# Kernel tuning notes

Measured on AMD Instinct MI355X. Metric: run time of the kernel, lower is better.

## Reference

```python
import jax, jax.numpy as jnp
import numpy as np

B, T, H, I, O, R = 64, 1024, 1024, 8, 8, 4
NOISE_STD, ALPHA = 0.05, 0.2


def setup_inputs() -> dict:
    key = jax.random.key(0)
    ks = jax.random.split(key, 6)
    return {
        "x": jax.random.normal(ks[0], (B, T, I), jnp.float32),
        "noise": jax.random.normal(ks[1], (B, T, H), jnp.float32),
        "wi": jax.random.normal(ks[2], (I, H), jnp.float32),
        "si": jnp.ones((I,), jnp.float32),
        "m": jax.random.normal(ks[3], (H, R), jnp.float32),
        "n": jax.random.normal(ks[4], (H, R), jnp.float32),
        "b": jnp.zeros((H,), jnp.float32),
        "wo": jax.random.normal(ks[5], (H, O), jnp.float32) / H,
        "so": jnp.ones((O,), jnp.float32),
        "h0": jnp.zeros((H,), jnp.float32),
    }


def reference(x, noise, wi, si, m, n, b, wo, so, h0):
    hidden = h0.shape[0]
    batch = x.shape[0]
    wi_full = wi * si[:, None]          # (I, H): (wi.T * si).T
    wo_full = wo * so                   # (H, O)
    h_init = jnp.broadcast_to(h0, (batch, hidden))
    r_init = jnp.tanh(h_init)           # non_linearity(initial_states)
    # precompute input drive for all steps: (B,T,H) -> scan over time-major
    u = jnp.einsum('bti,ih->tbh', x, wi_full)
    noise_t = jnp.transpose(noise, (1, 0, 2))  # (T,B,H)

    def step(carry, inp):
        h, r = carry
        u_i, nz_i = inp
        rec = (r @ n) @ m.T / hidden                    # low-rank recurrence
        h = h + NOISE_STD * nz_i + ALPHA * (-h + rec + u_i)
        r = jnp.tanh(h + b)
        out = h @ wo_full                               # identity output nonlin
        return (h, r), out

    _, outs = jax.lax.scan(step, (h_init, r_init), (u, noise_t))
    return jnp.transpose(outs, (1, 0, 2))  # (B,T,O)
```

## Files before the change

kernel.cpp:

```cpp
#include <hip/hip_runtime.h>

#define BB 64
#define TT 1024
#define HH 1024
#define II 8
#define OO 8
#define RRK 4
#define NOISE_STD 0.05f
#define ALPHA 0.2f

typedef float v4f __attribute__((ext_vector_type(4)));

#define C2E 2.885390081777927f

template<int CTRL, int RM>
__device__ __forceinline__ float dpp_add(float acc, float src) {
    int s = __builtin_amdgcn_update_dpp(0, __float_as_int(src), CTRL, RM, 0xF, true);
    return acc + __int_as_float(s);
}

__device__ __forceinline__ float wave_sum(float x) {
    x = dpp_add<0xB1, 0xF>(x, x);
    x = dpp_add<0x4E, 0xF>(x, x);
    x = dpp_add<0x141, 0xF>(x, x);
    x = dpp_add<0x140, 0xF>(x, x);
    x = dpp_add<0x142, 0xA>(x, x);
    x = dpp_add<0x143, 0xC>(x, x);
    return x;
}

__device__ __forceinline__ float rl63(float x) {
    return __int_as_float(__builtin_amdgcn_readlane(__float_as_int(x), 63));
}

__device__ __forceinline__ float tanh_from_l2x(float l2x) {
    float e = __builtin_amdgcn_exp2f(l2x);
    float r = __builtin_amdgcn_rcpf(e + 1.0f);
    return fmaf(-2.0f, r, 1.0f);
}

__device__ __forceinline__ void block_sync_lds() {
    asm volatile("s_waitcnt lgkmcnt(0)\n\ts_barrier" ::: "memory");
}

__device__ __forceinline__ void lds_fence() {
    asm volatile("s_waitcnt lgkmcnt(0)" ::: "memory");
}


__global__ __launch_bounds__(256)
void pre_d_kernel(const float* __restrict__ x, const float* __restrict__ noise,
                  const float* __restrict__ wi, const float* __restrict__ si,
                  const float* __restrict__ wo, const float* __restrict__ so,
                  float* __restrict__ d, float* __restrict__ sbase) {
    __shared__ __align__(16) float red[2][8][4][8];

    const int tid  = threadIdx.x;
    const int wave = tid >> 6;
    const int lane = tid & 63;
    const int e0   = tid << 2;

    v4f wia4[II];
    #pragma unroll
    for (int i = 0; i < II; ++i)
        wia4[i] = (ALPHA * si[i]) * *(const v4f*)(wi + (size_t)i * HH + e0);

    float woa[4][OO];
    #pragma unroll
    for (int e = 0; e < 4; ++e) {
        const float4 a4 = *(const float4*)(wo + (e0 + e) * OO);
        const float4 b4 = *(const float4*)(wo + (e0 + e) * OO + 4);
        woa[e][0] = a4.x * so[0]; woa[e][1] = a4.y * so[1];
        woa[e][2] = a4.z * so[2]; woa[e][3] = a4.w * so[3];
        woa[e][4] = b4.x * so[4]; woa[e][5] = b4.y * so[5];
        woa[e][6] = b4.z * so[6]; woa[e][7] = b4.w * so[7];
    }

    const int row0 = blockIdx.x * 32;
    float4 nz[8], nzn[8];
    #pragma unroll
    for (int j = 0; j < 8; ++j)
        nz[j] = *(const float4*)(noise + (size_t)(row0 + j) * HH + e0);

    #pragma unroll
    for (int ph = 0; ph < 4; ++ph) {
        const int cur   = ph & 1;
        const int rbase = row0 + ph * 8;

        if (ph < 3) {
            #pragma unroll
            for (int j = 0; j < 8; ++j)
                nzn[j] = *(const float4*)(noise + (size_t)(rbase + 8 + j) * HH + e0);
        }

        #pragma unroll
        for (int j = 0; j < 8; ++j) {
            const int row = rbase + j;
            const float4 xr0 = *(const float4*)(x + (size_t)row * II);
            const float4 xr1 = *(const float4*)(x + (size_t)row * II + 4);
            v4f u = xr0.x * wia4[0];
            u += xr0.y * wia4[1];  u += xr0.z * wia4[2];
            u += xr0.w * wia4[3];  u += xr1.x * wia4[4];
            u += xr1.y * wia4[5];  u += xr1.z * wia4[6];
            u += xr1.w * wia4[7];
            v4f d4 = u;
            d4.x = fmaf(NOISE_STD, nz[j].x, d4.x);
            d4.y = fmaf(NOISE_STD, nz[j].y, d4.y);
            d4.z = fmaf(NOISE_STD, nz[j].z, d4.z);
            d4.w = fmaf(NOISE_STD, nz[j].w, d4.w);
            *(v4f*)(d + (size_t)row * HH + e0) = d4;

            float op[OO];
            #pragma unroll
            for (int o = 0; o < OO; ++o)
                op[o] = fmaf(d4.x, woa[0][o], fmaf(d4.y, woa[1][o],
                        fmaf(d4.z, woa[2][o], d4.w * woa[3][o])));
            #pragma unroll
            for (int o = 0; o < OO; ++o) op[o] = wave_sum(op[o]);
            if (lane == 63) {
                *(float4*)&red[cur][j][wave][0] = make_float4(op[0], op[1], op[2], op[3]);
                *(float4*)&red[cur][j][wave][4] = make_float4(op[4], op[5], op[6], op[7]);
            }
        }
        block_sync_lds();
        if (tid < 64) {
            const int j = tid >> 3, o = tid & 7;
            sbase[(rbase + j) * OO + o] = (red[cur][j][0][o] + red[cur][j][1][o]) +
                                          (red[cur][j][2][o] + red[cur][j][3][o]);
        }
        #pragma unroll
        for (int j = 0; j < 8; ++j) nz[j] = nzn[j];
    }
}

__global__ __launch_bounds__(64, 1)
void rnn_d_kernel(const float* __restrict__ d, const float* __restrict__ sbase,
                  const float* __restrict__ mM, const float* __restrict__ nM,
                  const float* __restrict__ bv, const float* __restrict__ wo,
                  const float* __restrict__ so, const float* __restrict__ h0,
                  float* __restrict__ out) {
    __shared__ __align__(16) float lds_sb[TT * OO];
    __shared__ __align__(16) float lds_v[TT * RRK];
    __shared__ __align__(16) float amy[40];
    __shared__ float chs[8][OO];

    const int lane = threadIdx.x;
    const int b    = blockIdx.x;
    const int e0   = lane << 4;
    const int oc   = lane & 7;

    {
        const float4* ss = (const float4*)(sbase + (size_t)b * (TT * OO));
        float4* dsb = (float4*)lds_sb;
        #pragma unroll
        for (int k = 0; k < 32; ++k)
            dsb[k * 64 + lane] = ss[k * 64 + lane];
    }

    v4f mag[4][RRK];
    {
        const float cs = ALPHA / (float)HH;
        #pragma unroll
        for (int g = 0; g < 4; ++g) {
            v4f m0 = cs * *(const v4f*)(mM + (size_t)(e0 + g*4 + 0) * RRK);
            v4f m1 = cs * *(const v4f*)(mM + (size_t)(e0 + g*4 + 1) * RRK);
            v4f m2 = cs * *(const v4f*)(mM + (size_t)(e0 + g*4 + 2) * RRK);
            v4f m3 = cs * *(const v4f*)(mM + (size_t)(e0 + g*4 + 3) * RRK);
            #pragma unroll
            for (int q = 0; q < RRK; ++q)
                mag[g][q] = (v4f){m0[q], m1[q], m2[q], m3[q]};
        }
    }
    v4f h[4], r[4], tb[4];
    #pragma unroll
    for (int g = 0; g < 4; ++g) {
        h[g]  = *(const v4f*)(h0 + e0 + g * 4);
        tb[g] = C2E * *(const v4f*)(bv + e0 + g * 4);
        const v4f tg = C2E * h[g];
        r[g].x = tanh_from_l2x(tg.x); r[g].y = tanh_from_l2x(tg.y);
        r[g].z = tanh_from_l2x(tg.z); r[g].w = tanh_from_l2x(tg.w);
    }

    {
        float acc[40];
        #pragma unroll
        for (int k = 0; k < 40; ++k) acc[k] = 0.0f;
        float so8[OO];
        #pragma unroll
        for (int o = 0; o < OO; ++o) so8[o] = so[o];
        #pragma unroll
        for (int e = 0; e < 16; ++e) {
            const int g = e >> 2, eg = e & 3;
            const float4 a4 = *(const float4*)(wo + (size_t)(e0 + e) * OO);
            const float4 b4 = *(const float4*)(wo + (size_t)(e0 + e) * OO + 4);
            float wp[OO];
            wp[0] = a4.x * so8[0]; wp[1] = a4.y * so8[1];
            wp[2] = a4.z * so8[2]; wp[3] = a4.w * so8[3];
            wp[4] = b4.x * so8[4]; wp[5] = b4.y * so8[5];
            wp[6] = b4.z * so8[6]; wp[7] = b4.w * so8[7];
            #pragma unroll
            for (int q = 0; q < RRK; ++q) {
                const float ms = mag[g][q][eg];
                #pragma unroll
                for (int o = 0; o < OO; ++o)
                    acc[q * 8 + o] = fmaf(ms, wp[o], acc[q * 8 + o]);
            }
            const float hs = h[g][eg];
            #pragma unroll
            for (int o = 0; o < OO; ++o)
                acc[32 + o] = fmaf(hs, wp[o], acc[32 + o]);
        }
        #pragma unroll
        for (int k = 0; k < 40; ++k) acc[k] = wave_sum(acc[k]);
        if (lane == 63) {
            #pragma unroll
            for (int k = 0; k < 10; ++k)
                *(float4*)&amy[k * 4] = make_float4(acc[k*4+0], acc[k*4+1],
                                                    acc[k*4+2], acc[k*4+3]);
        }
    }

    v4f nrv[16];
    #pragma unroll
    for (int e = 0; e < 16; ++e)
        nrv[e] = *(const v4f*)(nM + (size_t)(e0 + e) * RRK);

    const float* dp = d + (size_t)b * (TT * HH) + e0;
    v4f dA[4], dB[4];
    #pragma unroll
    for (int g = 0; g < 4; ++g) {
        dA[g] = *(const v4f*)(dp + g * 4);
        dB[g] = *(const v4f*)(dp + (size_t)HH + g * 4);
    }

#define RNN_STEP(t, D, PF)                                                     \
    {                                                                          \
                  \
        v4f c0 = r[0].x * nrv[0];  c0 += r[0].y * nrv[1];                      \
        c0 += r[0].z * nrv[2];     c0 += r[0].w * nrv[3];                      \
        v4f c1 = r[1].x * nrv[4];  c1 += r[1].y * nrv[5];                      \
        c1 += r[1].z * nrv[6];     c1 += r[1].w * nrv[7];                      \
        v4f c2 = r[2].x * nrv[8];  c2 += r[2].y * nrv[9];                      \
        c2 += r[2].z * nrv[10];    c2 += r[2].w * nrv[11];                     \
        v4f c3 = r[3].x * nrv[12]; c3 += r[3].y * nrv[13];                     \
        c3 += r[3].z * nrv[14];    c3 += r[3].w * nrv[15];                     \
        const v4f vp = (c0 + c1) + (c2 + c3);                                  \
             \
        const float s0 = wave_sum(vp.x);                                       \
        const float s1 = wave_sum(vp.y);                                       \
        const float s2 = wave_sum(vp.z);                                       \
        const float s3 = wave_sum(vp.w);                                       \
        if (lane == 63)                                                        \
            *(float4*)&lds_v[(t) * RRK] = make_float4(s0, s1, s2, s3);         \
        const float v0 = rl63(s0);                                             \
        const float v1 = rl63(s1);                                             \
        const float v2 = rl63(s2);                                             \
        const float v3 = rl63(s3);                                             \
          \
        _Pragma("unroll")                                                      \
        for (int g = 0; g < 4; ++g) {                                          \
            v4f a = D[g];                                                      \
            a += v0 * mag[g][0];   a += v1 * mag[g][1];                        \
            a += v2 * mag[g][2];   a += v3 * mag[g][3];                        \
            h[g] = (1.0f - ALPHA) * h[g] + a;                                  \
        }                                                                      \
                     \
        if (PF) {                                                              \
            const float* np = dp + (size_t)((t) + 2) * HH;                     \
            _Pragma("unroll")                                                  \
            for (int g = 0; g < 4; ++g) D[g] = *(const v4f*)(np + g * 4);      \
        }                                                                      \
                                                          \
        _Pragma("unroll")                                                      \
        for (int g = 0; g < 4; ++g) {                                          \
            const v4f tg = C2E * h[g] + tb[g];                                 \
            r[g].x = tanh_from_l2x(tg.x); r[g].y = tanh_from_l2x(tg.y);        \
            r[g].z = tanh_from_l2x(tg.z); r[g].w = tanh_from_l2x(tg.w);        \
        }                                                                      \
    }

    for (int t = 0; t < TT - 2; t += 2) {
        RNN_STEP(t,     dA, 1)
        RNN_STEP(t + 1, dB, 1)
    }
    RNN_STEP(TT - 2, dA, 0)
    RNN_STEP(TT - 1, dB, 0)
#undef RNN_STEP

    lds_fence();

    float Amr[RRK];
    #pragma unroll
    for (int q = 0; q < RRK; ++q) Amr[q] = amy[q * 8 + oc];

    const int c  = lane >> 3;
    const int tc = c * 128;
    float a128;
    {
        float a = 1.0f - ALPHA;
        #pragma unroll
        for (int k = 0; k < 7; ++k) a = a * a;
        a128 = a;
    }

    auto step_s = [&](int t) -> float {
        const v4f vv = *(const v4f*)&lds_v[t * RRK];
        float s = lds_sb[t * OO + oc];
        s = fmaf(vv.x, Amr[0], s); s = fmaf(vv.y, Amr[1], s);
        s = fmaf(vv.z, Amr[2], s); s = fmaf(vv.w, Amr[3], s);
        return s;
    };

    float L = 0.0f;
    #pragma unroll 4
    for (int jt = 0; jt < 128; ++jt)
        L = fmaf(1.0f - ALPHA, L, step_s(tc + jt));
    chs[c][oc] = L;
    lds_fence();
    if (lane < OO) {
        float Y = amy[32 + lane];
        #pragma unroll
        for (int c2 = 0; c2 < 8; ++c2) {
            const float Lc = chs[c2][lane];
            chs[c2][lane] = Y;
            Y = fmaf(a128, Y, Lc);
        }
    }
    lds_fence();
    float yv = chs[c][oc];
    float* ob = out + (size_t)b * (TT * OO);
    #pragma unroll 4
    for (int jt = 0; jt < 128; ++jt) {
        const int t = tc + jt;
        yv = fmaf(1.0f - ALPHA, yv, step_s(t));
        ob[t * OO + oc] = yv;
    }
}


__global__ __launch_bounds__(256)
void prew_fb(const float* __restrict__ noise, const float* __restrict__ wo,
             const float* __restrict__ so, float* __restrict__ W) {
    __shared__ __align__(16) float red[2][8][4][8];

    const int tid  = threadIdx.x;
    const int wave = tid >> 6;
    const int lane = tid & 63;
    const int e0   = tid << 2;

    float woa[4][OO];
    {
        float so8[OO];
        #pragma unroll
        for (int o = 0; o < OO; ++o) so8[o] = so[o] * NOISE_STD;
        #pragma unroll
        for (int e = 0; e < 4; ++e) {
            const float4 a4 = *(const float4*)(wo + (e0 + e) * OO);
            const float4 b4 = *(const float4*)(wo + (e0 + e) * OO + 4);
            woa[e][0] = a4.x * so8[0]; woa[e][1] = a4.y * so8[1];
            woa[e][2] = a4.z * so8[2]; woa[e][3] = a4.w * so8[3];
            woa[e][4] = b4.x * so8[4]; woa[e][5] = b4.y * so8[5];
            woa[e][6] = b4.z * so8[6]; woa[e][7] = b4.w * so8[7];
        }
    }

    const int row0 = blockIdx.x * 32;
    float4 nz[8], nzn[8];
    #pragma unroll
    for (int j = 0; j < 8; ++j)
        nz[j] = *(const float4*)(noise + (size_t)(row0 + j) * HH + e0);

    #pragma unroll
    for (int ph = 0; ph < 4; ++ph) {
        const int cur   = ph & 1;
        const int rbase = row0 + ph * 8;
        if (ph < 3) {
            #pragma unroll
            for (int j = 0; j < 8; ++j)
                nzn[j] = *(const float4*)(noise + (size_t)(rbase + 8 + j) * HH + e0);
        }
        #pragma unroll
        for (int j = 0; j < 8; ++j) {
            float op[OO];
            #pragma unroll
            for (int o = 0; o < OO; ++o)
                op[o] = fmaf(nz[j].x, woa[0][o], fmaf(nz[j].y, woa[1][o],
                        fmaf(nz[j].z, woa[2][o], nz[j].w * woa[3][o])));
            #pragma unroll
            for (int o = 0; o < OO; ++o) op[o] = wave_sum(op[o]);
            if (lane == 63) {
                *(float4*)&red[cur][j][wave][0] = make_float4(op[0], op[1], op[2], op[3]);
                *(float4*)&red[cur][j][wave][4] = make_float4(op[4], op[5], op[6], op[7]);
            }
        }
        block_sync_lds();
        if (tid < 64) {
            const int j = tid >> 3, o = tid & 7;
            W[(rbase + j) * OO + o] = (red[cur][j][0][o] + red[cur][j][1][o]) +
                                      (red[cur][j][2][o] + red[cur][j][3][o]);
        }
        #pragma unroll
        for (int j = 0; j < 8; ++j) nz[j] = nzn[j];
    }
}

__global__ __launch_bounds__(256, 1)
void rnn_fb(const float* __restrict__ x, const float* __restrict__ noise,
            const float* __restrict__ wi, const float* __restrict__ si,
            const float* __restrict__ mM, const float* __restrict__ nM,
            const float* __restrict__ bv, const float* __restrict__ wo,
            const float* __restrict__ so, const float* __restrict__ h0,
            const float* __restrict__ W, float* __restrict__ out) {
    __shared__ __align__(16) float lds_x[(TT + 1) * II];
    __shared__ __align__(16) float lds_W[TT * OO];
    __shared__ __align__(16) float lds_out[TT * OO];
    __shared__ __align__(16) float red[4][4][4];
    __shared__ __align__(16) float redc[4][104];
    __shared__ float ambx[104];

    const int tid  = threadIdx.x;
    const int b    = blockIdx.x;
    const int wave = tid >> 6;
    const int lane = tid & 63;
    const int e0   = tid << 2;
    const int oc   = tid & 7;

    {
        const float4* sx = (const float4*)(x + (size_t)b * (TT * II));
        const float4* sw = (const float4*)(W + (size_t)b * (TT * OO));
        float4* dx = (float4*)lds_x;
        float4* dw = (float4*)lds_W;
        #pragma unroll
        for (int k = 0; k < 8; ++k) {
            dx[k * 256 + tid] = sx[k * 256 + tid];
            dw[k * 256 + tid] = sw[k * 256 + tid];
        }
        if (tid < 2) dx[2048 + tid] = sx[2046 + tid];
    }

    float wia[II][4];
    v4f   wiac[II];
    #pragma unroll
    for (int i = 0; i < II; ++i) {
        const float s  = ALPHA * si[i];
        const float4 w = *(const float4*)(wi + i * HH + e0);
        wia[i][0] = w.x * s; wia[i][1] = w.y * s; wia[i][2] = w.z * s; wia[i][3] = w.w * s;
        wiac[i] = (v4f){wia[i][0], wia[i][1], wia[i][2], wia[i][3]};
    }
    float ma[4][RRK];
    v4f   nrv[4];
    v4f   mac[RRK];
    #pragma unroll
    for (int e = 0; e < 4; ++e) {
        const float4 m4 = *(const float4*)(mM + (e0 + e) * RRK);
        const float4 n4 = *(const float4*)(nM + (e0 + e) * RRK);
        const float cs = ALPHA / (float)HH;
        ma[e][0] = m4.x * cs; ma[e][1] = m4.y * cs; ma[e][2] = m4.z * cs; ma[e][3] = m4.w * cs;
        nrv[e] = (v4f){n4.x, n4.y, n4.z, n4.w};
    }
    #pragma unroll
    for (int q = 0; q < RRK; ++q)
        mac[q] = (v4f){ma[0][q], ma[1][q], ma[2][q], ma[3][q]};

    float woa[4][OO];
    {
        #pragma unroll
        for (int e = 0; e < 4; ++e) {
            const float4 a4 = *(const float4*)(wo + (e0 + e) * OO);
            const float4 b4 = *(const float4*)(wo + (e0 + e) * OO + 4);
            woa[e][0] = a4.x * so[0]; woa[e][1] = a4.y * so[1];
            woa[e][2] = a4.z * so[2]; woa[e][3] = a4.w * so[3];
            woa[e][4] = b4.x * so[4]; woa[e][5] = b4.y * so[5];
            woa[e][6] = b4.z * so[6]; woa[e][7] = b4.w * so[7];
        }
    }
    v4f tb2e, h, rr;
    {
        const v4f b4 = *(const v4f*)(bv + e0);
        tb2e = C2E * b4;
        h = *(const v4f*)(h0 + e0);
        v4f targ = C2E * h;
        rr.x = tanh_from_l2x(targ.x); rr.y = tanh_from_l2x(targ.y);
        rr.z = tanh_from_l2x(targ.z); rr.w = tanh_from_l2x(targ.w);
    }

    #pragma unroll
    for (int kg = 0; kg < 26; ++kg) {
        float p[4];
        #pragma unroll
        for (int u = 0; u < 4; ++u) {
            const int k = kg * 4 + u;
            float s;
            if (k < 32) {
                const int q = k >> 3, o = k & 7;
                s = fmaf(ma[0][q], woa[0][o], fmaf(ma[1][q], woa[1][o],
                    fmaf(ma[2][q], woa[2][o], ma[3][q] * woa[3][o])));
            } else if (k < 96) {
                const int i = (k - 32) >> 3, o = k & 7;
                s = fmaf(wia[i][0], woa[0][o], fmaf(wia[i][1], woa[1][o],
                    fmaf(wia[i][2], woa[2][o], wia[i][3] * woa[3][o])));
            } else {
                const int o = k - 96;
                s = fmaf(h.x, woa[0][o], fmaf(h.y, woa[1][o],
                    fmaf(h.z, woa[2][o], h.w * woa[3][o])));
            }
            p[u] = wave_sum(s);
        }
        if (lane == 63)
            *(float4*)&redc[wave][kg * 4] = make_float4(p[0], p[1], p[2], p[3]);
    }
    block_sync_lds();
    if (tid < 104)
        ambx[tid] = (redc[0][tid] + redc[1][tid]) + (redc[2][tid] + redc[3][tid]);
    __syncthreads();

    float Amr[RRK], Bxr[II], y;
    #pragma unroll
    for (int q = 0; q < RRK; ++q) Amr[q] = ambx[q * 8 + oc];
    #pragma unroll
    for (int i = 0; i < II; ++i) Bxr[i] = ambx[32 + i * 8 + oc];
    y = ambx[96 + oc];

    const float* nzp = noise + (size_t)b * (TT * HH) + e0;
    v4f nzb[4];
    #pragma unroll
    for (int j = 0; j < 4; ++j) nzb[j] = *(const v4f*)(nzp + j * HH);

    v4f xqc0 = *(const v4f*)&lds_x[0];
    v4f xqc1 = *(const v4f*)&lds_x[4];
    float wqc = lds_W[oc];

    for (int t0 = 0; t0 < TT; t0 += 4) {
        #pragma unroll
        for (int j = 0; j < 4; ++j) {
            const int t = t0 + j;
            const int tn = t + 1;
            const v4f xqn0 = *(const v4f*)&lds_x[tn * II];
            const v4f xqn1 = *(const v4f*)&lds_x[tn * II + 4];
            const float wqn = lds_W[(tn & (TT - 1)) * OO + oc];

            v4f vpv = rr.x * nrv[0];
            vpv += rr.y * nrv[1];
            vpv += rr.z * nrv[2];
            vpv += rr.w * nrv[3];
            float vp0 = wave_sum(vpv.x);
            float vp1 = wave_sum(vpv.y);
            float vp2 = wave_sum(vpv.z);
            float vp3 = wave_sum(vpv.w);
            if (lane == 63)
                *(float4*)&red[j][wave][0] = make_float4(vp0, vp1, vp2, vp3);

            float ybase = fmaf(xqc0.x, Bxr[0], wqc);
            ybase = fmaf(xqc0.y, Bxr[1], ybase);
            ybase = fmaf(xqc0.z, Bxr[2], ybase);
            ybase = fmaf(xqc0.w, Bxr[3], ybase);
            ybase = fmaf(xqc1.x, Bxr[4], ybase);
            ybase = fmaf(xqc1.y, Bxr[5], ybase);
            ybase = fmaf(xqc1.z, Bxr[6], ybase);
            ybase = fmaf(xqc1.w, Bxr[7], ybase);

            v4f auv = xqc0.x * wiac[0];
            auv += xqc0.y * wiac[1];
            auv += xqc0.z * wiac[2];
            auv += xqc0.w * wiac[3];
            auv += xqc1.x * wiac[4];
            auv += xqc1.y * wiac[5];
            auv += xqc1.z * wiac[6];
            auv += xqc1.w * wiac[7];

            block_sync_lds();

            const v4f s0 = *(const v4f*)&red[j][0][0];
            const v4f s1 = *(const v4f*)&red[j][1][0];
            const v4f s2 = *(const v4f*)&red[j][2][0];
            const v4f s3 = *(const v4f*)&red[j][3][0];
            const v4f vs = (s0 + s1) + (s2 + s3);

            v4f acc = auv;
            acc += vs.x * mac[0];
            acc += vs.y * mac[1];
            acc += vs.z * mac[2];
            acc += vs.w * mac[3];
            h = (1.0f - ALPHA) * h + acc;
            h += NOISE_STD * nzb[j];

            {
                float t4 = fmaf(vs.x, Amr[0], ybase);
                t4 = fmaf(vs.y, Amr[1], t4);
                t4 = fmaf(vs.z, Amr[2], t4);
                t4 = fmaf(vs.w, Amr[3], t4);
                y = fmaf(1.0f - ALPHA, y, t4);
                if (tid < OO) lds_out[t * OO + tid] = y;
            }

            nzb[j] = *(const v4f*)(nzp + ((t + 4) & (TT - 1)) * HH);

            {
                v4f targ = C2E * h + tb2e;
                rr.x = tanh_from_l2x(targ.x);
                rr.y = tanh_from_l2x(targ.y);
                rr.z = tanh_from_l2x(targ.z);
                rr.w = tanh_from_l2x(targ.w);
            }
            xqc0 = xqn0; xqc1 = xqn1; wqc = wqn;
        }
    }

    __syncthreads();
    {
        float4* dst = (float4*)(out + (size_t)b * (TT * OO));
        const float4* srcv = (const float4*)lds_out;
        #pragma unroll
        for (int k = 0; k < 8; ++k)
            dst[k * 256 + tid] = srcv[k * 256 + tid];
    }
}

extern "C" void kernel_launch(void* const* d_in, const int* in_sizes, int n_in,
                              void* d_out, int out_size, void* d_ws, size_t ws_size,
                              hipStream_t stream) {
    const float* x     = (const float*)d_in[0];
    const float* noise = (const float*)d_in[1];
    const float* wi    = (const float*)d_in[2];
    const float* si    = (const float*)d_in[3];
    const float* mM    = (const float*)d_in[4];
    const float* nM    = (const float*)d_in[5];
    const float* bv    = (const float*)d_in[6];
    const float* wo    = (const float*)d_in[7];
    const float* so    = (const float*)d_in[8];
    const float* h0    = (const float*)d_in[9];
    float* out = (float*)d_out;

    const size_t needD = (size_t)BB * TT * HH * sizeof(float);
    const size_t needS = (size_t)BB * TT * OO * sizeof(float);

    if (ws_size >= needD + needS) {
        float* dbuf = (float*)d_ws;
        float* sb   = dbuf + (size_t)BB * TT * HH;
        pre_d_kernel<<<dim3(2048), dim3(256), 0, stream>>>(
            x, noise, wi, si, wo, so, dbuf, sb);
        rnn_d_kernel<<<dim3(BB), dim3(64), 0, stream>>>(
            dbuf, sb, mM, nM, bv, wo, so, h0, out);
    } else {
        float* W = (float*)d_ws;
        prew_fb<<<dim3(2048), dim3(256), 0, stream>>>(noise, wo, so, W);
        rnn_fb<<<dim3(BB), dim3(256), 0, stream>>>(
            x, noise, wi, si, mM, nM, bv, wo, so, h0, W, out);
    }
}
```

Measured before the change: 932.7 us.

## Split each batch's recurrence across four waves with per-step LDS reduction

```diff
diff --git a/kernel.cpp b/kernel.cpp
--- a/kernel.cpp
+++ b/kernel.cpp
@@ -29,10 +29,6 @@
     return x;
 }
 
-__device__ __forceinline__ float rl63(float x) {
-    return __int_as_float(__builtin_amdgcn_readlane(__float_as_int(x), 63));
-}
-
 __device__ __forceinline__ float tanh_from_l2x(float l2x) {
     float e = __builtin_amdgcn_exp2f(l2x);
     float r = __builtin_amdgcn_rcpf(e + 1.0f);
@@ -41,10 +37,6 @@
 
 __device__ __forceinline__ void block_sync_lds() {
     asm volatile("s_waitcnt lgkmcnt(0)\n\ts_barrier" ::: "memory");
-}
-
-__device__ __forceinline__ void lds_fence() {
-    asm volatile("s_waitcnt lgkmcnt(0)" ::: "memory");
 }
 
 
@@ -133,179 +125,158 @@
     }
 }
 
-__global__ __launch_bounds__(64, 1)
-void rnn_d_kernel(const float* __restrict__ d, const float* __restrict__ sbase,
-                  const float* __restrict__ mM, const float* __restrict__ nM,
-                  const float* __restrict__ bv, const float* __restrict__ wo,
-                  const float* __restrict__ so, const float* __restrict__ h0,
-                  float* __restrict__ out) {
-    __shared__ __align__(16) float lds_sb[TT * OO];
-    __shared__ __align__(16) float lds_v[TT * RRK];
+__global__ __launch_bounds__(512, 1)
+void rnn_pair(const float* __restrict__ d, const float* __restrict__ sbase,
+              const float* __restrict__ mM, const float* __restrict__ nM,
+              const float* __restrict__ bv, const float* __restrict__ wo,
+              const float* __restrict__ so, const float* __restrict__ h0,
+              float* __restrict__ out) {
+    __shared__ __align__(16) float lds_v[2][TT * RRK];
+    __shared__ __align__(16) float red[2][4][4][RRK];
+    __shared__ __align__(16) float redc[8][40];
     __shared__ __align__(16) float amy[40];
-    __shared__ float chs[8][OO];
-
-    const int lane = threadIdx.x;
-    const int b    = blockIdx.x;
-    const int e0   = lane << 4;
-    const int oc   = lane & 7;
-
-    {
-        const float4* ss = (const float4*)(sbase + (size_t)b * (TT * OO));
-        float4* dsb = (float4*)lds_sb;
-        #pragma unroll
-        for (int k = 0; k < 32; ++k)
-            dsb[k * 64 + lane] = ss[k * 64 + lane];
-    }
-
-    v4f mag[4][RRK];
-    {
+    __shared__ __align__(16) float chs[2][32][OO];
+
+    const int tid  = threadIdx.x;
+    const int wave = tid >> 6;
+    const int lane = tid & 63;
+    const int sg   = wave >> 2;
+    const int rw   = wave & 3;
+    const int tl   = tid & 255;
+    const int b    = blockIdx.x * 2 + sg;
+    const int hb   = rw * 256 + lane * 4;
+    const int oc   = tid & 7;
+
+    {
+        const int e2 = tid << 1;
         const float cs = ALPHA / (float)HH;
-        #pragma unroll
-        for (int g = 0; g < 4; ++g) {
-            v4f m0 = cs * *(const v4f*)(mM + (size_t)(e0 + g*4 + 0) * RRK);
-            v4f m1 = cs * *(const v4f*)(mM + (size_t)(e0 + g*4 + 1) * RRK);
-            v4f m2 = cs * *(const v4f*)(mM + (size_t)(e0 + g*4 + 2) * RRK);
-            v4f m3 = cs * *(const v4f*)(mM + (size_t)(e0 + g*4 + 3) * RRK);
+        const v4f m0 = cs * *(const v4f*)(mM + (size_t)e2 * RRK);
+        const v4f m1 = cs * *(const v4f*)(mM + (size_t)(e2 + 1) * RRK);
+        float wp0[OO], wp1[OO];
+        {
+            const float4 a4 = *(const float4*)(wo + (size_t)e2 * OO);
+            const float4 b4 = *(const float4*)(wo + (size_t)e2 * OO + 4);
+            wp0[0] = a4.x * so[0]; wp0[1] = a4.y * so[1];
+            wp0[2] = a4.z * so[2]; wp0[3] = a4.w * so[3];
+            wp0[4] = b4.x * so[4]; wp0[5] = b4.y * so[5];
+            wp0[6] = b4.z * so[6]; wp0[7] = b4.w * so[7];
+            const float4 c4 = *(const float4*)(wo + (size_t)(e2 + 1) * OO);
+            const float4 d4 = *(const float4*)(wo + (size_t)(e2 + 1) * OO + 4);
+            wp1[0] = c4.x * so[0]; wp1[1] = c4.y * so[1];
+            wp1[2] = c4.z * so[2]; wp1[3] = c4.w * so[3];
+            wp1[4] = d4.x * so[4]; wp1[5] = d4.y * so[5];
+            wp1[6] = d4.z * so[6]; wp1[7] = d4.w * so[7];
+        }
+        const float ha = h0[e2], hc = h0[e2 + 1];
+        #pragma unroll
+        for (int kg = 0; kg < 10; ++kg) {
+            float p[4];
             #pragma unroll
-            for (int q = 0; q < RRK; ++q)
-                mag[g][q] = (v4f){m0[q], m1[q], m2[q], m3[q]};
-        }
-    }
-    v4f h[4], r[4], tb[4];
-    #pragma unroll
-    for (int g = 0; g < 4; ++g) {
-        h[g]  = *(const v4f*)(h0 + e0 + g * 4);
-        tb[g] = C2E * *(const v4f*)(bv + e0 + g * 4);
-        const v4f tg = C2E * h[g];
-        r[g].x = tanh_from_l2x(tg.x); r[g].y = tanh_from_l2x(tg.y);
-        r[g].z = tanh_from_l2x(tg.z); r[g].w = tanh_from_l2x(tg.w);
-    }
-
-    {
-        float acc[40];
-        #pragma unroll
-        for (int k = 0; k < 40; ++k) acc[k] = 0.0f;
-        float so8[OO];
-        #pragma unroll
-        for (int o = 0; o < OO; ++o) so8[o] = so[o];
-        #pragma unroll
-        for (int e = 0; e < 16; ++e) {
-            const int g = e >> 2, eg = e & 3;
-            const float4 a4 = *(const float4*)(wo + (size_t)(e0 + e) * OO);
-            const float4 b4 = *(const float4*)(wo + (size_t)(e0 + e) * OO + 4);
-            float wp[OO];
-            wp[0] = a4.x * so8[0]; wp[1] = a4.y * so8[1];
-            wp[2] = a4.z * so8[2]; wp[3] = a4.w * so8[3];
-            wp[4] = b4.x * so8[4]; wp[5] = b4.y * so8[5];
-            wp[6] = b4.z * so8[6]; wp[7] = b4.w * so8[7];
-            #pragma unroll
-            for (int q = 0; q < RRK; ++q) {
-                const float ms = mag[g][q][eg];
-                #pragma unroll
-                for (int o = 0; o < OO; ++o)
-                    acc[q * 8 + o] = fmaf(ms, wp[o], acc[q * 8 + o]);
+            for (int u = 0; u < 4; ++u) {
+                const int k = kg * 4 + u;
+                float s;
+                if (k < 32) {
+                    const int q = k >> 3, o = k & 7;
+                    s = fmaf(m0[q], wp0[o], m1[q] * wp1[o]);
+                } else {
+                    const int o = k - 32;
+                    s = fmaf(ha, wp0[o], hc * wp1[o]);
+                }
+                p[u] = wave_sum(s);
             }
-            const float hs = h[g][eg];
-            #pragma unroll
-            for (int o = 0; o < OO; ++o)
-                acc[32 + o] = fmaf(hs, wp[o], acc[32 + o]);
-        }
-        #pragma unroll
-        for (int k = 0; k < 40; ++k) acc[k] = wave_sum(acc[k]);
-        if (lane == 63) {
-            #pragma unroll
-            for (int k = 0; k < 10; ++k)
-                *(float4*)&amy[k * 4] = make_float4(acc[k*4+0], acc[k*4+1],
-                                                    acc[k*4+2], acc[k*4+3]);
-        }
-    }
-
-    v4f nrv[16];
-    #pragma unroll
-    for (int e = 0; e < 16; ++e)
-        nrv[e] = *(const v4f*)(nM + (size_t)(e0 + e) * RRK);
-
-    const float* dp = d + (size_t)b * (TT * HH) + e0;
-    v4f dA[4], dB[4];
-    #pragma unroll
-    for (int g = 0; g < 4; ++g) {
-        dA[g] = *(const v4f*)(dp + g * 4);
-        dB[g] = *(const v4f*)(dp + (size_t)HH + g * 4);
-    }
-
-#define RNN_STEP(t, D, PF)                                                     \
-    {                                                                          \
-                  \
-        v4f c0 = r[0].x * nrv[0];  c0 += r[0].y * nrv[1];                      \
-        c0 += r[0].z * nrv[2];     c0 += r[0].w * nrv[3];                      \
-        v4f c1 = r[1].x * nrv[4];  c1 += r[1].y * nrv[5];                      \
-        c1 += r[1].z * nrv[6];     c1 += r[1].w * nrv[7];                      \
-        v4f c2 = r[2].x * nrv[8];  c2 += r[2].y * nrv[9];                      \
-        c2 += r[2].z * nrv[10];    c2 += r[2].w * nrv[11];                     \
-        v4f c3 = r[3].x * nrv[12]; c3 += r[3].y * nrv[13];                     \
-        c3 += r[3].z * nrv[14];    c3 += r[3].w * nrv[15];                     \
-        const v4f vp = (c0 + c1) + (c2 + c3);                                  \
-             \
-        const float s0 = wave_sum(vp.x);                                       \
-        const float s1 = wave_sum(vp.y);                                       \
-        const float s2 = wave_sum(vp.z);                                       \
-        const float s3 = wave_sum(vp.w);                                       \
-        if (lane == 63)                                                        \
-            *(float4*)&lds_v[(t) * RRK] = make_float4(s0, s1, s2, s3);         \
-        const float v0 = rl63(s0);                                             \
-        const float v1 = rl63(s1);                                             \
-        const float v2 = rl63(s2);                                             \
-        const float v3 = rl63(s3);                                             \
-          \
-        _Pragma("unroll")                                                      \
-        for (int g = 0; g < 4; ++g) {                                          \
-            v4f a = D[g];                                                      \
-            a += v0 * mag[g][0];   a += v1 * mag[g][1];                        \
-            a += v2 * mag[g][2];   a += v3 * mag[g][3];                        \
-            h[g] = (1.0f - ALPHA) * h[g] + a;                                  \
-        }                                                                      \
-                     \
-        if (PF) {                                                              \
-            const float* np = dp + (size_t)((t) + 2) * HH;                     \
-            _Pragma("unroll")                                                  \
-            for (int g = 0; g < 4; ++g) D[g] = *(const v4f*)(np + g * 4);      \
-        }                                                                      \
-                                                          \
-        _Pragma("unroll")                                                      \
-        for (int g = 0; g < 4; ++g) {                                          \
-            const v4f tg = C2E * h[g] + tb[g];                                 \
-            r[g].x = tanh_from_l2x(tg.x); r[g].y = tanh_from_l2x(tg.y);        \
-            r[g].z = tanh_from_l2x(tg.z); r[g].w = tanh_from_l2x(tg.w);        \
-        }                                                                      \
-    }
-
-    for (int t = 0; t < TT - 2; t += 2) {
-        RNN_STEP(t,     dA, 1)
-        RNN_STEP(t + 1, dB, 1)
-    }
-    RNN_STEP(TT - 2, dA, 0)
-    RNN_STEP(TT - 1, dB, 0)
-#undef RNN_STEP
-
-    lds_fence();
+            if (lane == 63)
+                *(float4*)&redc[wave][kg * 4] = make_float4(p[0], p[1], p[2], p[3]);
+        }
+    }
+    block_sync_lds();
+    if (tid < 40)
+        amy[tid] = ((redc[0][tid] + redc[1][tid]) + (redc[2][tid] + redc[3][tid])) +
+                   ((redc[4][tid] + redc[5][tid]) + (redc[6][tid] + redc[7][tid]));
+
+    v4f nrv[4], mac[RRK], h, r, tb2;
+    {
+        const float cs = ALPHA / (float)HH;
+        v4f mrow[4];
+        #pragma unroll
+        for (int e = 0; e < 4; ++e) {
+            nrv[e]  = *(const v4f*)(nM + (size_t)(hb + e) * RRK);
+            mrow[e] = cs * *(const v4f*)(mM + (size_t)(hb + e) * RRK);
+        }
+        #pragma unroll
+        for (int q = 0; q < RRK; ++q)
+            mac[q] = (v4f){mrow[0][q], mrow[1][q], mrow[2][q], mrow[3][q]};
+        h   = *(const v4f*)(h0 + hb);
+        tb2 = C2E * *(const v4f*)(bv + hb);
+        const v4f tg = C2E * h;
+        r.x = tanh_from_l2x(tg.x); r.y = tanh_from_l2x(tg.y);
+        r.z = tanh_from_l2x(tg.z); r.w = tanh_from_l2x(tg.w);
+    }
+
+    const float* dp = d + (size_t)b * (TT * HH) + hb;
+    v4f dbuf[4];
+    #pragma unroll
+    for (int j = 0; j < 4; ++j)
+        dbuf[j] = *(const v4f*)(dp + (size_t)j * HH);
+
+    for (int t0 = 0; t0 < TT; t0 += 4) {
+        #pragma unroll
+        for (int j = 0; j < 4; ++j) {
+            const int t = t0 + j;
+
+            v4f vp = r.x * nrv[0];
+            vp += r.y * nrv[1];
+            vp += r.z * nrv[2];
+            vp += r.w * nrv[3];
+            const float s0 = wave_sum(vp.x);
+            const float s1 = wave_sum(vp.y);
+            const float s2 = wave_sum(vp.z);
+            const float s3 = wave_sum(vp.w);
+            if (lane == 63)
+                *(float4*)&red[sg][j][rw][0] = make_float4(s0, s1, s2, s3);
+
+            block_sync_lds();
+
+            const v4f p0 = *(const v4f*)&red[sg][j][0][0];
+            const v4f p1 = *(const v4f*)&red[sg][j][1][0];
+            const v4f p2 = *(const v4f*)&red[sg][j][2][0];
+            const v4f p3 = *(const v4f*)&red[sg][j][3][0];
+            const v4f vs = (p0 + p1) + (p2 + p3);
+            if (tl == 0) *(v4f*)&lds_v[sg][t * RRK] = vs;
+
+            v4f acc = dbuf[j];
+            acc += vs.x * mac[0];
+            acc += vs.y * mac[1];
+            acc += vs.z * mac[2];
+            acc += vs.w * mac[3];
+            h = (1.0f - ALPHA) * h + acc;
+
+            dbuf[j] = *(const v4f*)(dp + (size_t)((t + 4) & (TT - 1)) * HH);
+
+            const v4f tg = C2E * h + tb2;
+            r.x = tanh_from_l2x(tg.x); r.y = tanh_from_l2x(tg.y);
+            r.z = tanh_from_l2x(tg.z); r.w = tanh_from_l2x(tg.w);
+        }
+    }
+
+    __syncthreads();
 
     float Amr[RRK];
     #pragma unroll
     for (int q = 0; q < RRK; ++q) Amr[q] = amy[q * 8 + oc];
 
-    const int c  = lane >> 3;
-    const int tc = c * 128;
-    float a128;
+    const int c  = tl >> 3;
+    const int tc = c * 32;
+    float a32;
     {
         float a = 1.0f - ALPHA;
-        #pragma unroll
-        for (int k = 0; k < 7; ++k) a = a * a;
-        a128 = a;
-    }
+        a = a * a; a = a * a; a = a * a; a = a * a; a = a * a;
+        a32 = a;
+    }
+    const float* sb = sbase + (size_t)b * (TT * OO);
 
     auto step_s = [&](int t) -> float {
-        const v4f vv = *(const v4f*)&lds_v[t * RRK];
-        float s = lds_sb[t * OO + oc];
+        const v4f vv = *(const v4f*)&lds_v[sg][t * RRK];
+        float s = sb[t * OO + oc];
         s = fmaf(vv.x, Amr[0], s); s = fmaf(vv.y, Amr[1], s);
         s = fmaf(vv.z, Amr[2], s); s = fmaf(vv.w, Amr[3], s);
         return s;
@@ -313,24 +284,24 @@
 
     float L = 0.0f;
     #pragma unroll 4
-    for (int jt = 0; jt < 128; ++jt)
+    for (int jt = 0; jt < 32; ++jt)
         L = fmaf(1.0f - ALPHA, L, step_s(tc + jt));
-    chs[c][oc] = L;
-    lds_fence();
-    if (lane < OO) {
-        float Y = amy[32 + lane];
-        #pragma unroll
-        for (int c2 = 0; c2 < 8; ++c2) {
-            const float Lc = chs[c2][lane];
-            chs[c2][lane] = Y;
-            Y = fmaf(a128, Y, Lc);
-        }
-    }
-    lds_fence();
-    float yv = chs[c][oc];
+    chs[sg][c][oc] = L;
+    block_sync_lds();
+    if (tl < OO) {
+        float Y = amy[32 + tl];
+        #pragma unroll 4
+        for (int c2 = 0; c2 < 32; ++c2) {
+            const float Lc = chs[sg][c2][tl];
+            chs[sg][c2][tl] = Y;
+            Y = fmaf(a32, Y, Lc);
+        }
+    }
+    block_sync_lds();
+    float yv = chs[sg][c][oc];
     float* ob = out + (size_t)b * (TT * OO);
     #pragma unroll 4
-    for (int jt = 0; jt < 128; ++jt) {
+    for (int jt = 0; jt < 32; ++jt) {
         const int t = tc + jt;
         yv = fmaf(1.0f - ALPHA, yv, step_s(t));
         ob[t * OO + oc] = yv;
@@ -639,7 +610,7 @@
         float* sb   = dbuf + (size_t)BB * TT * HH;
         pre_d_kernel<<<dim3(2048), dim3(256), 0, stream>>>(
             x, noise, wi, si, wo, so, dbuf, sb);
-        rnn_d_kernel<<<dim3(BB), dim3(64), 0, stream>>>(
+        rnn_pair<<<dim3(BB / 2), dim3(512), 0, stream>>>(
             dbuf, sb, mM, nM, bv, wo, so, h0, out);
     } else {
         float* W = (float*)d_ws;
```

Result: faster. 909.6 us (-2.5%).
